# Kernel optimization log

Measured on AMD Instinct MI355X. Metric: run time of the kernel, lower is better.

Reference implementation:

```python
import jax, jax.numpy as jnp
import numpy as np

N_NODES = 50000
N_EDGES = 800000
IN_CH = 256
HID = 512
OUT_CH = 1
N_GRAPHS = 64


def gcn_conv(x, W, b, src, dst, ew, n_nodes):
    # PyG GCNConv: x' = D^{-1/2} (A + I) D^{-1/2} (x W) + b, self-loop weight 1.0
    h = x @ W  # [N, F_out]
    deg = jax.ops.segment_sum(ew, dst, num_segments=n_nodes) + 1.0  # self loop adds 1
    dinv = jnp.where(deg > 0, jax.lax.rsqrt(deg), 0.0)
    norm = dinv[src] * ew * dinv[dst]  # [E]
    agg = jax.ops.segment_sum(h[src] * norm[:, None], dst, num_segments=n_nodes)
    agg = agg + h * (dinv * dinv)[:, None]  # self-loop contribution
    return agg + b


def global_mean_pool(x, batch, n_graphs):
    s = jax.ops.segment_sum(x, batch, num_segments=n_graphs)
    cnt = jax.ops.segment_sum(jnp.ones((x.shape[0],), x.dtype), batch, num_segments=n_graphs)
    return s / jnp.maximum(cnt, 1.0)[:, None]


def setup_inputs() -> dict:
    key = jax.random.key(0)
    ks = jax.random.split(key, 12)
    x = jax.random.normal(ks[0], (N_NODES, IN_CH), dtype=jnp.float32)
    edge_index = jax.random.randint(ks[1], (2, N_EDGES), 0, N_NODES, dtype=jnp.int64 if jax.config.jax_enable_x64 else jnp.int32)
    edge_weight = jax.random.uniform(ks[2], (N_EDGES,), dtype=jnp.float32)
    batch = jnp.sort(jax.random.randint(ks[3], (N_NODES,), 0, N_GRAPHS))
    # Glorot-ish init for params
    def glorot(k, fi, fo):
        return jax.random.normal(k, (fi, fo), dtype=jnp.float32) * np.float32(np.sqrt(2.0 / (fi + fo)))
    W1 = glorot(ks[4], IN_CH, HID)
    b1 = jnp.zeros((HID,), jnp.float32)
    W2 = glorot(ks[5], HID, HID)
    b2 = jnp.zeros((HID,), jnp.float32)
    Wl = glorot(ks[6], HID, OUT_CH)
    bl = jnp.zeros((OUT_CH,), jnp.float32)
    return {"x": x, "edge_index": edge_index, "edge_weight": edge_weight, "batch": batch,
            "W1": W1, "b1": b1, "W2": W2, "b2": b2, "Wl": Wl, "bl": bl}


def reference(x, edge_index, edge_weight, batch, W1, b1, W2, b2, Wl, bl):
    src, dst = edge_index[0], edge_index[1]
    h = gcn_conv(x, W1, b1, src, dst, edge_weight, N_NODES)
    h = jax.nn.relu(h)
    h = gcn_conv(h, W2, b2, src, dst, edge_weight, N_NODES)
    h = jax.nn.relu(h)
    g = global_mean_pool(h, batch, N_GRAPHS)  # [G, HID]
    return g @ Wl + bl  # [G, OUT_CH]
```

## Files before the change

### kernel.cpp

```cpp
#include <hip/hip_runtime.h>
#include <hip/hip_bf16.h>


#define N_NODES 50000
#define N_EDGES 800000
#define IN_CH   256
#define HID     512
#define N_GRAPHS 64
#define PDS     50048
#define NRB     391
#define MG_GRID 1568

typedef short bf16x8 __attribute__((ext_vector_type(8)));
typedef float f32x4  __attribute__((ext_vector_type(4)));

typedef const __attribute__((address_space(1))) void* gas_ptr;
typedef __attribute__((address_space(3))) void* las_ptr;

#define OFF_DEG    128
#define OFF_CNT    (OFF_DEG + N_NODES)
#define OFF_CURSOR (OFF_CNT + N_NODES)
#define ZERO_ELEMS (OFF_CURSOR + N_NODES)
#define OFF_DINV   ZERO_ELEMS
#define OFF_CSRPTR (OFF_DINV + N_NODES)
#define OFF_ESRC   (OFF_CSRPTR + N_NODES + 1)
#define OFF_ENORM  (OFF_ESRC + N_EDGES)
#define OFF_BT1H   1850368
#define OFF_BT1L   (OFF_BT1H + 65536)
#define OFF_BT2H   (OFF_BT1L + 65536)
#define OFF_BT2L   (OFF_BT2H + 131072)
#define OFF_PD     (OFF_BT2L + 131072)
#define OFF_XB     2643968
#define OFF_A      (OFF_XB + 6400000)
#define OFF_H1B    (OFF_A + 12800000)


static __device__ inline unsigned short f2bf(float f) {
    unsigned int u = __float_as_uint(f);
    return (unsigned short)((u + 0x7fff + ((u >> 16) & 1)) >> 16);
}
static __device__ inline float bf2f(unsigned short b) {
    return __uint_as_float(((unsigned int)b) << 16);
}
static __device__ inline void split_bf16(float v, unsigned short& hi, unsigned short& lo) {
    hi = f2bf(v);
    lo = f2bf(v - bf2f(hi));
}
static __device__ inline float bflo(unsigned int u) { return __uint_as_float(u << 16); }
static __device__ inline float bfhi(unsigned int u) { return __uint_as_float(u & 0xFFFF0000u); }


__global__ __launch_bounds__(256) void k_deg_cnt(const int* __restrict__ src,
                                                 const int* __restrict__ dst,
                                                 const float* __restrict__ ew,
                                                 float* __restrict__ deg,
                                                 int* __restrict__ cnt) {
    int e = blockIdx.x * blockDim.x + threadIdx.x;
    if (e >= N_EDGES) return;
    int d = dst[e];
    atomicAdd(&deg[d], ew[e]);
    atomicAdd(&cnt[d], 1);
}

__global__ __launch_bounds__(256) void k_dinv(const float* __restrict__ deg,
                                              float* __restrict__ dinv) {
    int i = blockIdx.x * blockDim.x + threadIdx.x;
    if (i >= N_NODES) return;
    dinv[i] = 1.0f / sqrtf(deg[i] + 1.0f);
}

__global__ __launch_bounds__(1024) void k_scan(const int* __restrict__ cnt,
                                               int* __restrict__ ptr, int n) {
    __shared__ int wsum[16];
    __shared__ int carry;
    int tid = threadIdx.x, lane = tid & 63, wid = tid >> 6;
    if (tid == 0) carry = 0;
    __syncthreads();
    for (int base = 0; base < n; base += 1024) {
        int i = base + tid;
        int v = (i < n) ? cnt[i] : 0;
        int incl = v;
        #pragma unroll
        for (int off = 1; off < 64; off <<= 1) {
            int t = __shfl_up(incl, off);
            if (lane >= off) incl += t;
        }
        if (lane == 63) wsum[wid] = incl;
        __syncthreads();
        if (tid == 0) {
            int run = carry;
            #pragma unroll
            for (int k = 0; k < 16; ++k) { int t = wsum[k]; wsum[k] = run; run += t; }
            carry = run;
        }
        __syncthreads();
        if (i < n) ptr[i] = wsum[wid] + incl - v;
        __syncthreads();
    }
    if (threadIdx.x == 0) ptr[n] = carry;
}

__global__ __launch_bounds__(256) void k_fill(const int* __restrict__ src,
                                              const int* __restrict__ dst,
                                              const float* __restrict__ ew,
                                              const float* __restrict__ dinv,
                                              const int* __restrict__ csrptr,
                                              int* __restrict__ cursor,
                                              int* __restrict__ esrc,
                                              float* __restrict__ enorm) {
    int e = blockIdx.x * blockDim.x + threadIdx.x;
    if (e >= N_EDGES) return;
    int s = src[e], d = dst[e];
    int pos = csrptr[d] + atomicAdd(&cursor[d], 1);
    esrc[pos] = s;
    enorm[pos] = dinv[s] * ew[e] * dinv[d];
}


template <int K>
__global__ __launch_bounds__(256) void k_convw(const float* __restrict__ W,
                                               unsigned short* __restrict__ BTh,
                                               unsigned short* __restrict__ BTl) {
    int idx = blockIdx.x * 256 + threadIdx.x;
    if (idx >= K * 512) return;
    int k = idx >> 9, n = idx & 511;
    unsigned short h, l;
    split_bf16(W[idx], h, l);
    BTh[(size_t)n * K + k] = h;
    BTl[(size_t)n * K + k] = l;
}

__global__ __launch_bounds__(256) void k_convx(const float* __restrict__ X,
                                               unsigned short* __restrict__ Xb, int n4) {
    int idx = blockIdx.x * 256 + threadIdx.x;
    if (idx >= n4) return;
    float4 v = ((const float4*)X)[idx];
    uint2 p;
    p.x = (unsigned int)f2bf(v.x) | ((unsigned int)f2bf(v.y) << 16);
    p.y = (unsigned int)f2bf(v.z) | ((unsigned int)f2bf(v.w) << 16);
    ((uint2*)Xb)[idx] = p;
}


template <int F>
__global__ __launch_bounds__(256) void k_agg(const unsigned short* __restrict__ X,
                                             const int* __restrict__ csrptr,
                                             const int* __restrict__ esrc,
                                             const float* __restrict__ enorm,
                                             const float* __restrict__ dinv,
                                             unsigned short* __restrict__ Yb) {
    constexpr int C = F / 64;
    constexpr int U = C / 2;
    int wave = (blockIdx.x * blockDim.x + threadIdx.x) >> 6;
    int lane = threadIdx.x & 63;
    if (wave >= N_NODES) return;
    int i = wave;
    float w0 = dinv[i] * dinv[i];
    float acc[C];
    {
        unsigned int u[U];
        const unsigned short* p = &X[(size_t)i * F + lane * C];
        if constexpr (U == 4) *(uint4*)u = *(const uint4*)p;
        else                  *(uint2*)u = *(const uint2*)p;
        #pragma unroll
        for (int j = 0; j < U; ++j) {
            acc[2 * j]     = w0 * bflo(u[j]);
            acc[2 * j + 1] = w0 * bfhi(u[j]);
        }
    }
    int s = csrptr[i], e = csrptr[i + 1];
    for (int j = s; j < e; ++j) {
        int sr = esrc[j];
        float w = enorm[j];
        unsigned int u[U];
        const unsigned short* p = &X[(size_t)sr * F + lane * C];
        if constexpr (U == 4) *(uint4*)u = *(const uint4*)p;
        else                  *(uint2*)u = *(const uint2*)p;
        #pragma unroll
        for (int q = 0; q < U; ++q) {
            acc[2 * q]     += w * bflo(u[q]);
            acc[2 * q + 1] += w * bfhi(u[q]);
        }
    }
    unsigned int pk[U];
    #pragma unroll
    for (int j = 0; j < U; ++j)
        pk[j] = (unsigned int)f2bf(acc[2 * j]) | ((unsigned int)f2bf(acc[2 * j + 1]) << 16);
    size_t base = (size_t)i * F + lane * C;
    if constexpr (U == 4) *(uint4*)&Yb[base] = *(uint4*)pk;
    else                  *(uint2*)&Yb[base] = *(uint2*)pk;
}

template <int K, bool DOT>
__global__ __launch_bounds__(256, 3) void k_mgemm(const unsigned short* __restrict__ Ab,
                                                  const unsigned short* __restrict__ BTh,
                                                  const unsigned short* __restrict__ BTl,
                                                  const float* __restrict__ bias,
                                                  unsigned short* __restrict__ Cb,
                                                  const float* __restrict__ Wl,
                                                  float* __restrict__ pd) {
    constexpr int NT = K / 32;
    __shared__ __align__(16) unsigned short smem[2 * 12288];

    int wgid = blockIdx.x;
    int rowblk = (wgid >> 5) * 8 + (wgid & 7);
    if (rowblk >= NRB) return;
    int colblk = (wgid >> 3) & 3;
    int tid = threadIdx.x, lane = tid & 63, wid = tid >> 6;
    int wm = wid >> 1, wn = wid & 1;
    int row0 = rowblk * 128 + wm * 64;
    int col0 = colblk * 128 + wn * 64;
    int l15 = lane & 15, l4 = lane >> 4;

    const unsigned short* gA;
    const unsigned short* gB = BTh;
    if (wid < 2) {
        int r = rowblk * 128 + wid * 64 + lane;
        if (r >= N_NODES) r = N_NODES - 1;
        gA = Ab + (size_t)r * K;
    } else {
        const unsigned short* mb = (wid == 2) ? BTh : BTl;
        gA = mb + (size_t)(colblk * 128 + lane) * K;
        gB = mb + (size_t)(colblk * 128 + 64 + lane) * K;
    }

    f32x4 acc[4][4];
    #pragma unroll
    for (int a = 0; a < 4; ++a)
        #pragma unroll
        for (int b = 0; b < 4; ++b) acc[a][b] = (f32x4){0.f, 0.f, 0.f, 0.f};

    auto STAGE = [&](int b) {
        unsigned short* lb = &smem[b * 12288];
        if (wid < 2) {
            #pragma unroll
            for (int g = 0; g < 4; ++g)
                __builtin_amdgcn_global_load_lds((gas_ptr)(gA + g * 8),
                                                 (las_ptr)(lb + g * 1024 + wid * 512), 16, 0, 0);
        } else {
            unsigned short* mb = lb + (wid - 1) * 4096;
            #pragma unroll
            for (int g = 0; g < 4; ++g) {
                __builtin_amdgcn_global_load_lds((gas_ptr)(gA + g * 8),
                                                 (las_ptr)(mb + g * 1024), 16, 0, 0);
                __builtin_amdgcn_global_load_lds((gas_ptr)(gB + g * 8),
                                                 (las_ptr)(mb + g * 1024 + 512), 16, 0, 0);
            }
        }
    };

    STAGE(0);
    __syncthreads();

    for (int t = 0; t < NT; ++t) {
        int cur = t & 1;
        if (t + 1 < NT) {
            gA += 32;
            if (wid >= 2) gB += 32;
            STAGE(cur ^ 1);
        }
        const unsigned short* sb = &smem[cur * 12288];
        int aoff = l4 * 1024 + (wm * 64 + l15) * 8;
        int boff = l4 * 1024 + (wn * 64 + l15) * 8;
        bf16x8 a[4];
        #pragma unroll
        for (int mf = 0; mf < 4; ++mf) a[mf] = *(const bf16x8*)&sb[aoff + mf * 128];
        #pragma unroll
        for (int nf = 0; nf < 4; ++nf) {
            bf16x8 bh = *(const bf16x8*)&sb[4096 + boff + nf * 128];
            bf16x8 bl = *(const bf16x8*)&sb[8192 + boff + nf * 128];
            #pragma unroll
            for (int mf = 0; mf < 4; ++mf) {
                acc[mf][nf] = __builtin_amdgcn_mfma_f32_16x16x32_bf16(a[mf], bh, acc[mf][nf], 0, 0, 0);
                acc[mf][nf] = __builtin_amdgcn_mfma_f32_16x16x32_bf16(a[mf], bl, acc[mf][nf], 0, 0, 0);
            }
        }
        __syncthreads();
    }

    if (!DOT) {
        #pragma unroll
        for (int mf = 0; mf < 4; ++mf)
            #pragma unroll
            for (int nf = 0; nf < 4; ++nf) {
                int c = col0 + nf * 16 + l15;
                float bv = bias[c];
                #pragma unroll
                for (int r = 0; r < 4; ++r) {
                    int row = row0 + mf * 16 + l4 * 4 + r;
                    if (row < N_NODES)
                        Cb[(size_t)row * 512 + c] = f2bf(fmaxf(acc[mf][nf][r] + bv, 0.f));
                }
            }
    } else {
        float rowsum[4][4];
        #pragma unroll
        for (int mf = 0; mf < 4; ++mf)
            #pragma unroll
            for (int r = 0; r < 4; ++r) rowsum[mf][r] = 0.f;
        #pragma unroll
        for (int nf = 0; nf < 4; ++nf) {
            int c = col0 + nf * 16 + l15;
            float bv = bias[c];
            float wv = Wl[c];
            #pragma unroll
            for (int mf = 0; mf < 4; ++mf)
                #pragma unroll
                for (int r = 0; r < 4; ++r)
                    rowsum[mf][r] += fmaxf(acc[mf][nf][r] + bv, 0.f) * wv;
        }
        #pragma unroll
        for (int mf = 0; mf < 4; ++mf)
            #pragma unroll
            for (int r = 0; r < 4; ++r) {
                float v = rowsum[mf][r];
                #pragma unroll
                for (int mask = 1; mask <= 8; mask <<= 1) v += __shfl_xor(v, mask);
                if (l15 == 0) {
                    int row = row0 + mf * 16 + l4 * 4 + r;
                    if (row < N_NODES)
                        pd[(size_t)(colblk * 2 + wn) * PDS + row] = v;
                }
            }
    }
}


__global__ __launch_bounds__(256) void k_gpool(const float* __restrict__ pd,
                                               const int* __restrict__ batch,
                                               const float* __restrict__ bl,
                                               float* __restrict__ out) {
    int g = blockIdx.x;
    int tid = threadIdx.x;
    float s = 0.f;
    int c = 0;
    for (int i = tid; i < N_NODES; i += 256) {
        if (batch[i] == g) {
            float v = 0.f;
            #pragma unroll
            for (int p = 0; p < 8; ++p) v += pd[(size_t)p * PDS + i];
            s += v;
            c += 1;
        }
    }
    __shared__ float ss[4];
    __shared__ int sc[4];
    int lane = tid & 63, wid = tid >> 6;
    #pragma unroll
    for (int off = 32; off > 0; off >>= 1) {
        s += __shfl_down(s, off);
        c += __shfl_down(c, off);
    }
    if (lane == 0) { ss[wid] = s; sc[wid] = c; }
    __syncthreads();
    if (tid == 0) {
        float S = ss[0] + ss[1] + ss[2] + ss[3];
        int C = sc[0] + sc[1] + sc[2] + sc[3];
        out[g] = S / fmaxf((float)C, 1.0f) + bl[0];
    }
}


extern "C" void kernel_launch(void* const* d_in, const int* in_sizes, int n_in,
                              void* d_out, int out_size, void* d_ws, size_t ws_size,
                              hipStream_t stream) {
    const float* x  = (const float*)d_in[0];
    const int* ei   = (const int*)d_in[1];
    const float* ew = (const float*)d_in[2];
    const int* batch= (const int*)d_in[3];
    const float* W1 = (const float*)d_in[4];
    const float* b1 = (const float*)d_in[5];
    const float* W2 = (const float*)d_in[6];
    const float* b2 = (const float*)d_in[7];
    const float* Wl = (const float*)d_in[8];
    const float* bl = (const float*)d_in[9];
    float* out = (float*)d_out;

    const int* src = ei;
    const int* dst = ei + N_EDGES;

    float* ws = (float*)d_ws;
    float* deg    = ws + OFF_DEG;
    int*   cnt    = (int*)(ws + OFF_CNT);
    int*   cursor = (int*)(ws + OFF_CURSOR);
    float* dinv   = ws + OFF_DINV;
    int*   csrptr = (int*)(ws + OFF_CSRPTR);
    int*   esrc   = (int*)(ws + OFF_ESRC);
    float* enorm  = ws + OFF_ENORM;
    unsigned short* bt1h = (unsigned short*)(ws + OFF_BT1H);
    unsigned short* bt1l = (unsigned short*)(ws + OFF_BT1L);
    unsigned short* bt2h = (unsigned short*)(ws + OFF_BT2H);
    unsigned short* bt2l = (unsigned short*)(ws + OFF_BT2L);
    float* pd     = ws + OFF_PD;
    unsigned short* xb  = (unsigned short*)(ws + OFF_XB);
    unsigned short* a1  = (unsigned short*)(ws + OFF_A);
    unsigned short* a2  = (unsigned short*)(ws + OFF_A);
    unsigned short* h1b = (unsigned short*)(ws + OFF_H1B);

    hipMemsetAsync(ws, 0, (size_t)ZERO_ELEMS * 4, stream);

    int eb = (N_EDGES + 255) / 256;
    int nb = (N_NODES + 255) / 256;
    int wb = (N_NODES * 64 + 255) / 256;

    k_deg_cnt<<<eb, 256, 0, stream>>>(src, dst, ew, deg, cnt);
    k_dinv<<<nb, 256, 0, stream>>>(deg, dinv);
    k_scan<<<1, 1024, 0, stream>>>(cnt, csrptr, N_NODES);
    k_fill<<<eb, 256, 0, stream>>>(src, dst, ew, dinv, csrptr, cursor, esrc, enorm);

    k_convw<IN_CH><<<(IN_CH * 512 + 255) / 256, 256, 0, stream>>>(W1, bt1h, bt1l);
    k_convw<HID><<<(HID * 512 + 255) / 256, 256, 0, stream>>>(W2, bt2h, bt2l);
    k_convx<<<(N_NODES * IN_CH / 4 + 255) / 256, 256, 0, stream>>>(x, xb, N_NODES * IN_CH / 4);

    k_agg<IN_CH><<<wb, 256, 0, stream>>>(xb, csrptr, esrc, enorm, dinv, a1);
    k_mgemm<IN_CH, false><<<MG_GRID, 256, 0, stream>>>(a1, bt1h, bt1l, b1, h1b, nullptr, nullptr);

    k_agg<HID><<<wb, 256, 0, stream>>>(h1b, csrptr, esrc, enorm, dinv, a2);
    k_mgemm<HID, true><<<MG_GRID, 256, 0, stream>>>(a2, bt2h, bt2l, b2, nullptr, Wl, pd);

    k_gpool<<<N_GRAPHS, 256, 0, stream>>>(pd, batch, bl, out);
}
```

Before: 778.7 us.

## Enlarge MFMA GEMM tile to 256 rows with 8-wave workgroups

The split-bf16 GEMM workgroup grows from 4 to 8 waves and covers 256 rows instead of 128, so each B tile (high and low parts) staged in LDS is reused across twice as many rows. Staging becomes uniform: four waves load A rows and four load the B hi/lo halves, with a larger double-buffered LDS area. This halves redundant B-matrix loads and the grid size, but increases LDS per block and may lower occupancy or leave imbalance from fewer workgroups. The epilogue is not shown changing, and 8 waves with wm = wid>>1 index rows 0-255, which looks consistent.

```diff
diff --git a/kernel.cpp b/kernel.cpp
--- a/kernel.cpp
+++ b/kernel.cpp
@@ -8,8 +8,8 @@
 #define HID     512
 #define N_GRAPHS 64
 #define PDS     50048
-#define NRB     391
-#define MG_GRID 1568
+#define NRB     196
+#define MG_GRID 800
 
 typedef short bf16x8 __attribute__((ext_vector_type(8)));
 typedef float f32x4  __attribute__((ext_vector_type(4)));
@@ -192,7 +192,7 @@
 }
 
 template <int K, bool DOT>
-__global__ __launch_bounds__(256, 3) void k_mgemm(const unsigned short* __restrict__ Ab,
+__global__ __launch_bounds__(512, 4) void k_mgemm(const unsigned short* __restrict__ Ab,
                                                   const unsigned short* __restrict__ BTh,
                                                   const unsigned short* __restrict__ BTl,
                                                   const float* __restrict__ bias,
@@ -200,7 +200,7 @@
                                                   const float* __restrict__ Wl,
                                                   float* __restrict__ pd) {
     constexpr int NT = K / 32;
-    __shared__ __align__(16) unsigned short smem[2 * 12288];
+    __shared__ __align__(16) unsigned short smem[2 * 16384];
 
     int wgid = blockIdx.x;
     int rowblk = (wgid >> 5) * 8 + (wgid & 7);
@@ -208,20 +208,25 @@
     int colblk = (wgid >> 3) & 3;
     int tid = threadIdx.x, lane = tid & 63, wid = tid >> 6;
     int wm = wid >> 1, wn = wid & 1;
-    int row0 = rowblk * 128 + wm * 64;
+    int row0 = rowblk * 256 + wm * 64;
     int col0 = colblk * 128 + wn * 64;
     int l15 = lane & 15, l4 = lane >> 4;
 
-    const unsigned short* gA;
-    const unsigned short* gB = BTh;
-    if (wid < 2) {
-        int r = rowblk * 128 + wid * 64 + lane;
+    const unsigned short* gS;
+    int ldsoff;
+    int gstride;
+    if (wid < 4) {
+        int r = rowblk * 256 + wid * 64 + lane;
         if (r >= N_NODES) r = N_NODES - 1;
-        gA = Ab + (size_t)r * K;
+        gS = Ab + (size_t)r * K;
+        ldsoff = wid * 512 + lane * 8;
+        gstride = 2048;
     } else {
-        const unsigned short* mb = (wid == 2) ? BTh : BTl;
-        gA = mb + (size_t)(colblk * 128 + lane) * K;
-        gB = mb + (size_t)(colblk * 128 + 64 + lane) * K;
+        int p = (wid - 4) >> 1, h = (wid - 4) & 1;
+        const unsigned short* mb = p ? BTl : BTh;
+        gS = mb + (size_t)(colblk * 128 + h * 64 + lane) * K;
+        ldsoff = 8192 + p * 4096 + h * 512 + lane * 8;
+        gstride = 1024;
     }
 
     f32x4 acc[4][4];
@@ -231,22 +236,12 @@
         for (int b = 0; b < 4; ++b) acc[a][b] = (f32x4){0.f, 0.f, 0.f, 0.f};
 
     auto STAGE = [&](int b) {
-        unsigned short* lb = &smem[b * 12288];
-        if (wid < 2) {
-            #pragma unroll
-            for (int g = 0; g < 4; ++g)
-                __builtin_amdgcn_global_load_lds((gas_ptr)(gA + g * 8),
-                                                 (las_ptr)(lb + g * 1024 + wid * 512), 16, 0, 0);
-        } else {
-            unsigned short* mb = lb + (wid - 1) * 4096;
-            #pragma unroll
-            for (int g = 0; g < 4; ++g) {
-                __builtin_amdgcn_global_load_lds((gas_ptr)(gA + g * 8),
-                                                 (las_ptr)(mb + g * 1024), 16, 0, 0);
-                __builtin_amdgcn_global_load_lds((gas_ptr)(gB + g * 8),
-                                                 (las_ptr)(mb + g * 1024 + 512), 16, 0, 0);
-            }
-        }
+        unsigned short* lb = &smem[b * 16384];
+        #pragma unroll
+        for (int g = 0; g < 4; ++g)
+            __builtin_amdgcn_global_load_lds((gas_ptr)(gS + g * 8),
+                                             (las_ptr)(lb + ldsoff - lane * 8 + g * gstride + lane * 8),
+                                             16, 0, 0);
     };
 
     STAGE(0);
@@ -255,20 +250,19 @@
     for (int t = 0; t < NT; ++t) {
         int cur = t & 1;
         if (t + 1 < NT) {
-            gA += 32;
-            if (wid >= 2) gB += 32;
+            gS += 32;
             STAGE(cur ^ 1);
         }
-        const unsigned short* sb = &smem[cur * 12288];
-        int aoff = l4 * 1024 + (wm * 64 + l15) * 8;
+        const unsigned short* sb = &smem[cur * 16384];
+        int aoff = l4 * 2048 + (wm * 64 + l15) * 8;
         int boff = l4 * 1024 + (wn * 64 + l15) * 8;
         bf16x8 a[4];
         #pragma unroll
         for (int mf = 0; mf < 4; ++mf) a[mf] = *(const bf16x8*)&sb[aoff + mf * 128];
         #pragma unroll
         for (int nf = 0; nf < 4; ++nf) {
-            bf16x8 bh = *(const bf16x8*)&sb[4096 + boff + nf * 128];
-            bf16x8 bl = *(const bf16x8*)&sb[8192 + boff + nf * 128];
+            bf16x8 bh = *(const bf16x8*)&sb[8192 + boff + nf * 128];
+            bf16x8 bl = *(const bf16x8*)&sb[12288 + boff + nf * 128];
             #pragma unroll
             for (int mf = 0; mf < 4; ++mf) {
                 acc[mf][nf] = __builtin_amdgcn_mfma_f32_16x16x32_bf16(a[mf], bh, acc[mf][nf], 0, 0, 0);
@@ -413,10 +407,10 @@
     k_convx<<<(N_NODES * IN_CH / 4 + 255) / 256, 256, 0, stream>>>(x, xb, N_NODES * IN_CH / 4);
 
     k_agg<IN_CH><<<wb, 256, 0, stream>>>(xb, csrptr, esrc, enorm, dinv, a1);
-    k_mgemm<IN_CH, false><<<MG_GRID, 256, 0, stream>>>(a1, bt1h, bt1l, b1, h1b, nullptr, nullptr);
+    k_mgemm<IN_CH, false><<<MG_GRID, 512, 0, stream>>>(a1, bt1h, bt1l, b1, h1b, nullptr, nullptr);
 
     k_agg<HID><<<wb, 256, 0, stream>>>(h1b, csrptr, esrc, enorm, dinv, a2);
-    k_mgemm<HID, true><<<MG_GRID, 256, 0, stream>>>(a2, bt2h, bt2l, b2, nullptr, Wl, pd);
+    k_mgemm<HID, true><<<MG_GRID, 512, 0, stream>>>(a2, bt2h, bt2l, b2, nullptr, Wl, pd);
 
     k_gpool<<<N_GRAPHS, 256, 0, stream>>>(pd, batch, bl, out);
 }
```

Measured after the change: 717.1 us. 1.09x faster.
